# Kernel optimization log

Hardware: AMD Instinct MI355X
Metric: run time of the kernel (lower is better)

The kernel has to match this reference:

```python
import jax, jax.numpy as jnp
import numpy as np

FMAP = 56    # feature-map side (seq_len = FMAP**2 = 3136)
WS = 7       # window size
SHIFT = WS // 2  # 3, shifted-window offset
NH = 3       # heads
C = 96       # hidden dim
FF = 384     # feed-forward dim (4*C)
EPS = 1e-5


def _swin_mask():
    # Standard Swin shifted-window attention mask, shape (nW, L, L), values in {0, -1e9}.
    img = np.zeros((FMAP, FMAP), dtype=np.int32)
    slices = (slice(0, -WS), slice(-WS, -SHIFT), slice(-SHIFT, None))
    cnt = 0
    for hs in slices:
        for ws_ in slices:
            img[hs, ws_] = cnt
            cnt += 1
    w = img.reshape(FMAP // WS, WS, FMAP // WS, WS).transpose(0, 2, 1, 3).reshape(-1, WS * WS)
    m = np.where(w[:, None, :] != w[:, :, None], -1e9, 0.0).astype(np.float32)
    return jnp.asarray(m)  # (nW, L, L)


def _ln(x, w, b):
    mu = jnp.mean(x, axis=-1, keepdims=True)
    var = jnp.mean(jnp.square(x - mu), axis=-1, keepdims=True)
    return (x - mu) * jax.lax.rsqrt(var + EPS) * w + b


def setup_inputs() -> dict:
    key = jax.random.key(0)
    ks = jax.random.split(key, 8)
    s = 0.02
    return {
        "x": jax.random.normal(ks[0], (128, FMAP * FMAP, C), dtype=jnp.float32),
        "qkv_w": jax.random.normal(ks[1], (3 * C, C), dtype=jnp.float32) * s,
        "qkv_b": jnp.zeros((3 * C,), dtype=jnp.float32),
        "out_w": jax.random.normal(ks[2], (C, C), dtype=jnp.float32) * s,
        "out_b": jnp.zeros((C,), dtype=jnp.float32),
        "ln1_w": jnp.ones((C,), dtype=jnp.float32),
        "ln1_b": jnp.zeros((C,), dtype=jnp.float32),
        "ln2_w": jnp.ones((C,), dtype=jnp.float32),
        "ln2_b": jnp.zeros((C,), dtype=jnp.float32),
        "ff1_w": jax.random.normal(ks[3], (FF, C), dtype=jnp.float32) * s,
        "ff1_b": jnp.zeros((FF,), dtype=jnp.float32),
        "ff2_w": jax.random.normal(ks[4], (C, FF), dtype=jnp.float32) * s,
        "ff2_b": jnp.zeros((C,), dtype=jnp.float32),
    }


def reference(x, qkv_w, qkv_b, out_w, out_b, ln1_w, ln1_b, ln2_w, ln2_b, ff1_w, ff1_b, ff2_w, ff2_b):
    B, S, Cd = x.shape
    L = WS * WS
    g = FMAP // WS
    nW = g * g
    hd = Cd // NH

    # cyclic shift + window partition: (B, S, C) -> (B*nW, L, C)
    xi = jnp.roll(x.reshape(B, FMAP, FMAP, Cd), (-SHIFT, -SHIFT), axis=(1, 2))
    xw = xi.reshape(B, g, WS, g, WS, Cd).transpose(0, 1, 3, 2, 4, 5).reshape(B * nW, L, Cd)

    mask = _swin_mask()                                  # (nW, L, L)
    mask = jnp.tile(mask, (B, 1, 1))[:, None, :, :]      # (B*nW, 1, L, L)

    # pre-norm MHA
    h = _ln(xw, ln1_w, ln1_b)
    qkv = h @ qkv_w.T + qkv_b
    q, k, v = jnp.split(qkv, 3, axis=-1)
    def heads(t):
        return t.reshape(B * nW, L, NH, hd).transpose(0, 2, 1, 3)  # (B*nW, H, L, hd)
    q, k, v = heads(q), heads(k), heads(v)
    scores = jnp.einsum('bhqd,bhkd->bhqk', q, k) / jnp.sqrt(jnp.float32(hd)) + mask
    attn = jax.nn.softmax(scores, axis=-1)
    o = jnp.einsum('bhqk,bhkd->bhqd', attn, v).transpose(0, 2, 1, 3).reshape(B * nW, L, Cd)
    xw = xw + o @ out_w.T + out_b

    # pre-norm FFN with exact (erf) GELU, as torch activation='gelu'
    h2 = _ln(xw, ln2_w, ln2_b)
    xw = xw + jax.nn.gelu(h2 @ ff1_w.T + ff1_b, approximate=False) @ ff2_w.T + ff2_b

    # window merge + reverse shift
    xo = xw.reshape(B, g, g, WS, WS, Cd).transpose(0, 1, 3, 2, 4, 5).reshape(B, FMAP, FMAP, Cd)
    xo = jnp.roll(xo, (SHIFT, SHIFT), axis=(1, 2))
    return xo.reshape(B, S, Cd)
```

## Files before the change

### kernel.cpp

```cpp
#include <hip/hip_runtime.h>
#include <stdint.h>

#define FMAPD 56
#define LD 49
#define CD 96

using u16 = unsigned short;
using u32 = unsigned int;

typedef __attribute__((ext_vector_type(8))) short bh8;
typedef __attribute__((ext_vector_type(4))) float f4;

__device__ __forceinline__ u16 f2b(float f) {
  union { float f; u32 i; } v; v.f = f;
  u32 r = v.i + 0x7fffu + ((v.i >> 16) & 1u);
  return (u16)(r >> 16);
}
__device__ __forceinline__ u32 pk2(float a, float b) {
  return (u32)f2b(a) | ((u32)f2b(b) << 16);
}

__device__ __forceinline__ float gelu_f(float v) {
  float x = fabsf(v) * 0.70710678118654752f;
  float t = __builtin_amdgcn_rcpf(fmaf(x, 0.3275911f, 1.0f));
  float p = fmaf(t, 1.061405429f, -1.453152027f);
  p = fmaf(p, t, 1.421413741f);
  p = fmaf(p, t, -0.284496736f);
  p = fmaf(p, t, 0.254829592f);
  p = p * t;
  float e = __expf(-x * x);
  float q = 0.5f * p * e;
  float phi = (v >= 0.0f) ? (1.0f - q) : q;
  return v * phi;
}

#define SH 104
#define SV 72
#define SP 104

__global__ void cvt_weights(const float* __restrict__ a, const float* __restrict__ b,
                            const float* __restrict__ c, const float* __restrict__ d,
                            u16* __restrict__ ws) {
  int i = blockIdx.x * 256 + threadIdx.x;
  if (i < 27648)       ws[i] = f2b(a[i]);
  else if (i < 36864)  ws[i] = f2b(b[i - 27648]);
  else if (i < 73728)  ws[i] = f2b(c[i - 36864]);
  else if (i < 110592) ws[i] = f2b(d[i - 73728]);
}

__global__ __launch_bounds__(256, 3)
void swin_mfma(const float* __restrict__ gx,
               const float* __restrict__ b_qkv,
               const float* __restrict__ b_out,
               const float* __restrict__ w_ln1, const float* __restrict__ b_ln1,
               const float* __restrict__ w_ln2, const float* __restrict__ b_ln2,
               const float* __restrict__ b_ff1, const float* __restrict__ b_ff2,
               const u16* __restrict__ ws,
               float* __restrict__ gout)
{
  __shared__ __align__(16) u16 s_h [64 * SH];
  __shared__ __align__(16) u16 s_k [64 * SH];
  __shared__ __align__(16) u16 s_vt[96 * SV];
  __shared__ __align__(16) u16 s_p [4 * 16 * SP];
  __shared__ __align__(16) int s_id[64];

  const int tid = threadIdx.x;
  const int w = tid >> 6, lane = tid & 63, g = lane >> 4, lq = lane & 15;
  const int blk = blockIdx.x, b = blk >> 6, wr = (blk >> 3) & 7, wc = blk & 7;

  const u16* wsq = ws;
  const u16* wso = ws + 27648;
  const u16* wf1 = ws + 36864;
  const u16* wf2 = ws + 73728;

  u16* s_pw = s_p + w * (16 * SP);

  if (tid < 64) {
    int id = -1;
    if (tid < 49) {
      int i = tid / 7, j = tid - 7 * i;
      int rp = wr * 7 + i, cp = wc * 7 + j;
      int ri = (rp < 49) ? 0 : ((rp < 53) ? 1 : 2);
      int ci = (cp < 49) ? 0 : ((cp < 53) ? 1 : 2);
      id = ri * 3 + ci;
    }
    s_id[tid] = id;
  }

  float resid[6][4];
  size_t gbase[4];
  bool tval[4];
#pragma unroll
  for (int r = 0; r < 4; ++r) {
    int token = 16 * w + 4 * g + r;
    tval[r] = token < LD;
    int ti = token / 7, tj = token - 7 * ti;
    int row = wr * 7 + ti + 3; if (row >= FMAPD) row -= FMAPD;
    int col = wc * 7 + tj + 3; if (col >= FMAPD) col -= FMAPD;
    gbase[r] = ((size_t)b * (FMAPD * FMAPD) + row * FMAPD + col) * (size_t)CD + lq;
#pragma unroll
    for (int t = 0; t < 6; ++t) {
      float v = gx[gbase[r] + 16 * t];
      resid[t][r] = tval[r] ? v : 0.f;
    }
  }

  float bq[6][4];
#pragma unroll
  for (int t = 0; t < 6; ++t) {
    float4 v = *(const float4*)(b_qkv + 16 * t + 4 * g);
    bq[t][0] = v.x; bq[t][1] = v.y; bq[t][2] = v.z; bq[t][3] = v.w;
  }
  float bvv[6], bov[6], bf2v[6];
#pragma unroll
  for (int t = 0; t < 6; ++t) {
    bvv[t]  = b_qkv[192 + 16 * t + lq];
    bov[t]  = b_out[16 * t + lq];
    bf2v[t] = b_ff2[16 * t + lq];
  }

  auto layer_norm = [&](const float* lw, const float* lb) {
    float wv[6], bv[6];
#pragma unroll
    for (int t = 0; t < 6; ++t) { wv[t] = lw[16 * t + lq]; bv[t] = lb[16 * t + lq]; }
#pragma unroll
    for (int r = 0; r < 4; ++r) {
      float s = 0.f, s2 = 0.f;
#pragma unroll
      for (int t = 0; t < 6; ++t) { float v = resid[t][r]; s += v; s2 += v * v; }
#pragma unroll
      for (int m = 1; m <= 8; m <<= 1) { s += __shfl_xor(s, m, 64); s2 += __shfl_xor(s2, m, 64); }
      float mu = s * (1.f / 96.f);
      float rs = rsqrtf(s2 * (1.f / 96.f) - mu * mu + 1e-5f);
      u16* dst = s_h + (16 * w + 4 * g + r) * SH;
#pragma unroll
      for (int t = 0; t < 6; ++t) dst[16 * t + lq] = f2b((resid[t][r] - mu) * rs * wv[t] + bv[t]);
    }
  };
  layer_norm(w_ln1, b_ln1);

  {
    const u16* arow = s_h + (16 * w + lq) * SH;
    bh8 af[3];
#pragma unroll
    for (int kk = 0; kk < 3; ++kk) af[kk] = *(const bh8*)(arow + 32 * kk + 8 * g);

#pragma unroll
    for (int t = 0; t < 6; ++t) {
      f4 acc = {0.f, 0.f, 0.f, 0.f};
#pragma unroll
      for (int kk = 0; kk < 3; ++kk) {
        bh8 bf = *(const bh8*)(wsq + (16 * t + lq) * CD + 32 * kk + 8 * g);
        acc = __builtin_amdgcn_mfma_f32_16x16x32_bf16(bf, af[kk], acc, 0, 0, 0);
      }
      uint2 u; u.x = pk2(acc[0] + bq[t][0], acc[1] + bq[t][1]);
      u.y = pk2(acc[2] + bq[t][2], acc[3] + bq[t][3]);
      *(uint2*)(s_pw + lq * SP + 16 * t + 4 * g) = u;
    }
#pragma unroll
    for (int t = 0; t < 6; ++t) {
      f4 acc = {0.f, 0.f, 0.f, 0.f};
#pragma unroll
      for (int kk = 0; kk < 3; ++kk) {
        bh8 bf = *(const bh8*)(wsq + (96 + 16 * t + lq) * CD + 32 * kk + 8 * g);
        acc = __builtin_amdgcn_mfma_f32_16x16x32_bf16(bf, af[kk], acc, 0, 0, 0);
      }
      uint2 u; u.x = pk2(acc[0], acc[1]); u.y = pk2(acc[2], acc[3]);
      *(uint2*)(s_k + (16 * w + lq) * SH + 16 * t + 4 * g) = u;
    }
#pragma unroll
    for (int t = 0; t < 6; ++t) {
      f4 acc = {0.f, 0.f, 0.f, 0.f};
#pragma unroll
      for (int kk = 0; kk < 3; ++kk) {
        bh8 bf = *(const bh8*)(wsq + (192 + 16 * t + lq) * CD + 32 * kk + 8 * g);
        acc = __builtin_amdgcn_mfma_f32_16x16x32_bf16(af[kk], bf, acc, 0, 0, 0);
      }
      float bias = bvv[t];
      uint2 u; u.x = pk2(acc[0] + bias, acc[1] + bias);
      u.y = pk2(acc[2] + bias, acc[3] + bias);
      *(uint2*)(s_vt + (16 * t + lq) * SV + 16 * w + 4 * g) = u;
    }
  }
  bh8 qa[3];
#pragma unroll
  for (int hh = 0; hh < 3; ++hh) qa[hh] = *(const bh8*)(s_pw + lq * SP + 32 * hh + 8 * g);

  __syncthreads();

  const int id_i = s_id[16 * w + lq];
  int idj[4][4];
#pragma unroll
  for (int t = 0; t < 4; ++t) {
    int4 v = *(const int4*)(s_id + 16 * t + 4 * g);
    idj[t][0] = v.x; idj[t][1] = v.y; idj[t][2] = v.z; idj[t][3] = v.w;
  }
  const float scale = 0.17677669529663687f;

#pragma unroll
  for (int hh = 0; hh < 3; ++hh) {
    f4 sc[4];
#pragma unroll
    for (int t = 0; t < 4; ++t) {
      bh8 kb = *(const bh8*)(s_k + (16 * t + lq) * SH + 32 * hh + 8 * g);
      f4 z = {0.f, 0.f, 0.f, 0.f};
      sc[t] = __builtin_amdgcn_mfma_f32_16x16x32_bf16(kb, qa[hh], z, 0, 0, 0);
    }
    float pv[4][4];
    float mx = -3.0e38f;
#pragma unroll
    for (int t = 0; t < 4; ++t)
#pragma unroll
      for (int r = 0; r < 4; ++r) {
        float v = sc[t][r] * scale;
        v = (id_i != idj[t][r]) ? v - 1e9f : v;
        pv[t][r] = v;
        mx = fmaxf(mx, v);
      }
    mx = fmaxf(mx, __shfl_xor(mx, 16, 64));
    mx = fmaxf(mx, __shfl_xor(mx, 32, 64));
    float den = 0.f;
#pragma unroll
    for (int t = 0; t < 4; ++t)
#pragma unroll
      for (int r = 0; r < 4; ++r) { float e = __expf(pv[t][r] - mx); pv[t][r] = e; den += e; }
    den += __shfl_xor(den, 16, 64);
    den += __shfl_xor(den, 32, 64);
    float inv = 1.0f / den;
#pragma unroll
    for (int t = 0; t < 4; ++t) {
      uint2 u; u.x = pk2(pv[t][0] * inv, pv[t][1] * inv);
      u.y = pk2(pv[t][2] * inv, pv[t][3] * inv);
      *(uint2*)(s_pw + lq * SP + 16 * t + 4 * g) = u;
    }
    bh8 pa0 = *(const bh8*)(s_pw + lq * SP + 8 * g);
    bh8 pa1 = *(const bh8*)(s_pw + lq * SP + 32 + 8 * g);
#pragma unroll
    for (int nt = 0; nt < 2; ++nt) {
      const u16* vrow = s_vt + (32 * hh + 16 * nt + lq) * SV;
      bh8 vb0 = *(const bh8*)(vrow + 8 * g);
      bh8 vb1 = *(const bh8*)(vrow + 32 + 8 * g);
      f4 o = {0.f, 0.f, 0.f, 0.f};
      o = __builtin_amdgcn_mfma_f32_16x16x32_bf16(vb0, pa0, o, 0, 0, 0);
      o = __builtin_amdgcn_mfma_f32_16x16x32_bf16(vb1, pa1, o, 0, 0, 0);
      uint2 u; u.x = pk2(o[0], o[1]); u.y = pk2(o[2], o[3]);
      *(uint2*)(s_h + (16 * w + lq) * SH + 32 * hh + 16 * nt + 4 * g) = u;
    }
  }

  {
    const u16* orow = s_h + (16 * w + lq) * SH;
    bh8 oa[3];
#pragma unroll
    for (int kk = 0; kk < 3; ++kk) oa[kk] = *(const bh8*)(orow + 32 * kk + 8 * g);
#pragma unroll
    for (int t = 0; t < 6; ++t) {
      f4 acc = {0.f, 0.f, 0.f, 0.f};
#pragma unroll
      for (int kk = 0; kk < 3; ++kk) {
        bh8 bf = *(const bh8*)(wso + (16 * t + lq) * CD + 32 * kk + 8 * g);
        acc = __builtin_amdgcn_mfma_f32_16x16x32_bf16(oa[kk], bf, acc, 0, 0, 0);
      }
#pragma unroll
      for (int r = 0; r < 4; ++r) resid[t][r] += acc[r] + bov[t];
    }
  }

  layer_norm(w_ln2, b_ln2);
#pragma unroll
  for (int t = 0; t < 6; ++t)
#pragma unroll
    for (int r = 0; r < 4; ++r) resid[t][r] += bf2v[t];

  __syncthreads();

  {
    const u16* hrow = s_h + (16 * w + lq) * SH;
    bh8 ha[3];
#pragma unroll
    for (int kk = 0; kk < 3; ++kk) ha[kk] = *(const bh8*)(hrow + 32 * kk + 8 * g);
    const u16* frow = s_k + (16 * w + lq) * SH;
#pragma unroll 1
    for (int qq = 0; qq < 4; ++qq) {
      float bq1[6][4];
#pragma unroll
      for (int t = 0; t < 6; ++t) {
        float4 v = *(const float4*)(b_ff1 + 96 * qq + 16 * t + 4 * g);
        bq1[t][0] = v.x; bq1[t][1] = v.y; bq1[t][2] = v.z; bq1[t][3] = v.w;
      }
#pragma unroll
      for (int t = 0; t < 6; ++t) {
        f4 acc = {0.f, 0.f, 0.f, 0.f};
#pragma unroll
        for (int kk = 0; kk < 3; ++kk) {
          bh8 bf = *(const bh8*)(wf1 + (96 * qq + 16 * t + lq) * CD + 32 * kk + 8 * g);
          acc = __builtin_amdgcn_mfma_f32_16x16x32_bf16(bf, ha[kk], acc, 0, 0, 0);
        }
        uint2 u;
        u.x = pk2(gelu_f(acc[0] + bq1[t][0]), gelu_f(acc[1] + bq1[t][1]));
        u.y = pk2(gelu_f(acc[2] + bq1[t][2]), gelu_f(acc[3] + bq1[t][3]));
        *(uint2*)(s_k + (16 * w + lq) * SH + 16 * t + 4 * g) = u;
      }
      bh8 fa[3];
#pragma unroll
      for (int ks = 0; ks < 3; ++ks) fa[ks] = *(const bh8*)(frow + 32 * ks + 8 * g);
#pragma unroll
      for (int t = 0; t < 6; ++t) {
        f4 acc = {0.f, 0.f, 0.f, 0.f};
#pragma unroll
        for (int ks = 0; ks < 3; ++ks) {
          bh8 bf = *(const bh8*)(wf2 + (16 * t + lq) * 384 + 96 * qq + 32 * ks + 8 * g);
          acc = __builtin_amdgcn_mfma_f32_16x16x32_bf16(fa[ks], bf, acc, 0, 0, 0);
        }
#pragma unroll
        for (int r = 0; r < 4; ++r) resid[t][r] += acc[r];
      }
    }
  }

#pragma unroll
  for (int r = 0; r < 4; ++r) {
    if (tval[r]) {
#pragma unroll
      for (int t = 0; t < 6; ++t) gout[gbase[r] + 16 * t] = resid[t][r];
    }
  }
}

extern "C" void kernel_launch(void* const* d_in, const int* in_sizes, int n_in,
                              void* d_out, int out_size, void* d_ws, size_t ws_size,
                              hipStream_t stream) {
  cvt_weights<<<432, 256, 0, stream>>>(
      (const float*)d_in[1], (const float*)d_in[3],
      (const float*)d_in[9], (const float*)d_in[11], (u16*)d_ws);
  swin_mfma<<<8192, 256, 0, stream>>>(
      (const float*)d_in[0],
      (const float*)d_in[2],
      (const float*)d_in[4],
      (const float*)d_in[5], (const float*)d_in[6],
      (const float*)d_in[7], (const float*)d_in[8],
      (const float*)d_in[10], (const float*)d_in[12],
      (const u16*)d_ws, (float*)d_out);
}
```

Before: 876.8 us.

## Transpose MFMA fragments in registers via permlane swaps instead of LDS round-trips

Q, attention probabilities, attention output and the FF1 activations are now turned into MFMA A-operands with an in-register 4x4 lane transpose (permlane32/16 swaps, with a shuffle fallback) instead of being written to and re-read from shared memory. The softmax drops its max-subtraction and uses exp2, with the scale and log2(e) folded into Q, and the mask becomes a precomputed additive table. GELU also uses exp2, shared buffers are merged so LDS use shrinks, and launch bounds go from 3 to 4 blocks per SM. Bias values are read at the point of use rather than held in registers. Skipping the max subtraction relies on scores staying small enough that exp2 does not overflow.

After: 815.9 us. 1.07x faster.

```diff
diff --git a/kernel.cpp b/kernel.cpp
--- a/kernel.cpp
+++ b/kernel.cpp
@@ -10,6 +10,7 @@
 
 typedef __attribute__((ext_vector_type(8))) short bh8;
 typedef __attribute__((ext_vector_type(4))) float f4;
+typedef __attribute__((ext_vector_type(2))) unsigned int uv2;
 
 __device__ __forceinline__ u16 f2b(float f) {
   union { float f; u32 i; } v; v.f = f;
@@ -19,6 +20,38 @@
 __device__ __forceinline__ u32 pk2(float a, float b) {
   return (u32)f2b(a) | ((u32)f2b(b) << 16);
 }
+__device__ __forceinline__ bh8 mk8(u32 a, u32 b, u32 c, u32 d) {
+  union { u32 u[4]; bh8 v; } x;
+  x.u[0] = a; x.u[1] = b; x.u[2] = c; x.u[3] = d;
+  return x.v;
+}
+__device__ __forceinline__ float ex2(float x) { return __builtin_amdgcn_exp2f(x); }
+
+#if __has_builtin(__builtin_amdgcn_permlane32_swap) && __has_builtin(__builtin_amdgcn_permlane16_swap)
+__device__ __forceinline__ void xpose4(u32& v0, u32& v1, u32& v2, u32& v3) {
+  uv2 a = __builtin_amdgcn_permlane32_swap(v0, v2, false, false);
+  uv2 b = __builtin_amdgcn_permlane32_swap(v1, v3, false, false);
+  uv2 c = __builtin_amdgcn_permlane16_swap(a.x, a.y, false, false);
+  uv2 d = __builtin_amdgcn_permlane16_swap(b.x, b.y, false, false);
+  v0 = c.x; v2 = c.y; v1 = d.x; v3 = d.y;
+}
+#else
+__device__ __forceinline__ void xpose4(u32& v0, u32& v1, u32& v2, u32& v3) {
+  int lane = threadIdx.x & 63;
+  { u32 t0 = __shfl_xor((int)v0, 32, 64), t2 = __shfl_xor((int)v2, 32, 64);
+    bool lo = (lane & 32) == 0;
+    u32 n0 = lo ? v0 : t2, n2 = lo ? t0 : v2; v0 = n0; v2 = n2; }
+  { u32 t1 = __shfl_xor((int)v1, 32, 64), t3 = __shfl_xor((int)v3, 32, 64);
+    bool lo = (lane & 32) == 0;
+    u32 n1 = lo ? v1 : t3, n3 = lo ? t1 : v3; v1 = n1; v3 = n3; }
+  { u32 t0 = __shfl_xor((int)v0, 16, 64), t2 = __shfl_xor((int)v2, 16, 64);
+    bool lo = (lane & 16) == 0;
+    u32 n0 = lo ? v0 : t2, n2 = lo ? t0 : v2; v0 = n0; v2 = n2; }
+  { u32 t1 = __shfl_xor((int)v1, 16, 64), t3 = __shfl_xor((int)v3, 16, 64);
+    bool lo = (lane & 16) == 0;
+    u32 n1 = lo ? v1 : t3, n3 = lo ? t1 : v3; v1 = n1; v3 = n3; }
+}
+#endif
 
 __device__ __forceinline__ float gelu_f(float v) {
   float x = fabsf(v) * 0.70710678118654752f;
@@ -28,7 +61,7 @@
   p = fmaf(p, t, -0.284496736f);
   p = fmaf(p, t, 0.254829592f);
   p = p * t;
-  float e = __expf(-x * x);
+  float e = ex2(v * v * -0.72134752044448170f);
   float q = 0.5f * p * e;
   float phi = (v >= 0.0f) ? (1.0f - q) : q;
   return v * phi;
@@ -36,7 +69,6 @@
 
 #define SH 104
 #define SV 72
-#define SP 104
 
 __global__ void cvt_weights(const float* __restrict__ a, const float* __restrict__ b,
                             const float* __restrict__ c, const float* __restrict__ d,
@@ -48,7 +80,7 @@
   else if (i < 110592) ws[i] = f2b(d[i - 73728]);
 }
 
-__global__ __launch_bounds__(256, 3)
+__global__ __launch_bounds__(256, 4)
 void swin_mfma(const float* __restrict__ gx,
                const float* __restrict__ b_qkv,
                const float* __restrict__ b_out,
@@ -58,10 +90,8 @@
                const u16* __restrict__ ws,
                float* __restrict__ gout)
 {
-  __shared__ __align__(16) u16 s_h [64 * SH];
-  __shared__ __align__(16) u16 s_k [64 * SH];
-  __shared__ __align__(16) u16 s_vt[96 * SV];
-  __shared__ __align__(16) u16 s_p [4 * 16 * SP];
+  __shared__ __align__(16) u16 s_u[96 * SV];
+  __shared__ __align__(16) u16 s_k[64 * SH];
   __shared__ __align__(16) int s_id[64];
 
   const int tid = threadIdx.x;
@@ -73,11 +103,9 @@
   const u16* wf1 = ws + 36864;
   const u16* wf2 = ws + 73728;
 
-  u16* s_pw = s_p + w * (16 * SP);
-
   if (tid < 64) {
     int id = -1;
-    if (tid < 49) {
+    if (tid < LD) {
       int i = tid / 7, j = tid - 7 * i;
       int rp = wr * 7 + i, cp = wc * 7 + j;
       int ri = (rp < 49) ? 0 : ((rp < 53) ? 1 : 2);
@@ -89,34 +117,19 @@
 
   float resid[6][4];
   size_t gbase[4];
-  bool tval[4];
 #pragma unroll
   for (int r = 0; r < 4; ++r) {
     int token = 16 * w + 4 * g + r;
-    tval[r] = token < LD;
     int ti = token / 7, tj = token - 7 * ti;
     int row = wr * 7 + ti + 3; if (row >= FMAPD) row -= FMAPD;
     int col = wc * 7 + tj + 3; if (col >= FMAPD) col -= FMAPD;
     gbase[r] = ((size_t)b * (FMAPD * FMAPD) + row * FMAPD + col) * (size_t)CD + lq;
+    bool val = token < LD;
 #pragma unroll
     for (int t = 0; t < 6; ++t) {
       float v = gx[gbase[r] + 16 * t];
-      resid[t][r] = tval[r] ? v : 0.f;
-    }
-  }
-
-  float bq[6][4];
-#pragma unroll
-  for (int t = 0; t < 6; ++t) {
-    float4 v = *(const float4*)(b_qkv + 16 * t + 4 * g);
-    bq[t][0] = v.x; bq[t][1] = v.y; bq[t][2] = v.z; bq[t][3] = v.w;
-  }
-  float bvv[6], bov[6], bf2v[6];
-#pragma unroll
-  for (int t = 0; t < 6; ++t) {
-    bvv[t]  = b_qkv[192 + 16 * t + lq];
-    bov[t]  = b_out[16 * t + lq];
-    bf2v[t] = b_ff2[16 * t + lq];
+      resid[t][r] = val ? v : 0.f;
+    }
   }
 
   auto layer_norm = [&](const float* lw, const float* lb) {
@@ -132,30 +145,44 @@
       for (int m = 1; m <= 8; m <<= 1) { s += __shfl_xor(s, m, 64); s2 += __shfl_xor(s2, m, 64); }
       float mu = s * (1.f / 96.f);
       float rs = rsqrtf(s2 * (1.f / 96.f) - mu * mu + 1e-5f);
-      u16* dst = s_h + (16 * w + 4 * g + r) * SH;
+      u16* dst = s_u + (16 * w + 4 * g + r) * SH;
 #pragma unroll
       for (int t = 0; t < 6; ++t) dst[16 * t + lq] = f2b((resid[t][r] - mu) * rs * wv[t] + bv[t]);
     }
   };
   layer_norm(w_ln1, b_ln1);
 
-  {
-    const u16* arow = s_h + (16 * w + lq) * SH;
-    bh8 af[3];
+  bh8 af[3];
+  {
+    const u16* arow = s_u + (16 * w + lq) * SH;
 #pragma unroll
     for (int kk = 0; kk < 3; ++kk) af[kk] = *(const bh8*)(arow + 32 * kk + 8 * g);
-
-#pragma unroll
-    for (int t = 0; t < 6; ++t) {
-      f4 acc = {0.f, 0.f, 0.f, 0.f};
-#pragma unroll
-      for (int kk = 0; kk < 3; ++kk) {
-        bh8 bf = *(const bh8*)(wsq + (16 * t + lq) * CD + 32 * kk + 8 * g);
-        acc = __builtin_amdgcn_mfma_f32_16x16x32_bf16(bf, af[kk], acc, 0, 0, 0);
-      }
-      uint2 u; u.x = pk2(acc[0] + bq[t][0], acc[1] + bq[t][1]);
-      u.y = pk2(acc[2] + bq[t][2], acc[3] + bq[t][3]);
-      *(uint2*)(s_pw + lq * SP + 16 * t + 4 * g) = u;
+  }
+  __syncthreads();
+
+  const float scaleL = 0.25505650948822f;
+  bh8 qa[3];
+  {
+#pragma unroll
+    for (int c = 0; c < 3; ++c) {
+      u32 vv[4];
+#pragma unroll
+      for (int j1 = 0; j1 < 2; ++j1) {
+        int t = 2 * c + j1;
+        f4 acc = {0.f, 0.f, 0.f, 0.f};
+#pragma unroll
+        for (int kk = 0; kk < 3; ++kk) {
+          bh8 bf = *(const bh8*)(wsq + (16 * t + lq) * CD + 32 * kk + 8 * g);
+          acc = __builtin_amdgcn_mfma_f32_16x16x32_bf16(bf, af[kk], acc, 0, 0, 0);
+        }
+        float4 bq = *(const float4*)(b_qkv + 16 * t + 4 * g);
+        vv[2 * j1 + 0] = pk2(fmaf(acc[0], scaleL, bq.x * scaleL),
+                             fmaf(acc[1], scaleL, bq.y * scaleL));
+        vv[2 * j1 + 1] = pk2(fmaf(acc[2], scaleL, bq.z * scaleL),
+                             fmaf(acc[3], scaleL, bq.w * scaleL));
+      }
+      xpose4(vv[0], vv[1], vv[2], vv[3]);
+      qa[c] = mk8(vv[0], vv[1], vv[2], vv[3]);
     }
 #pragma unroll
     for (int t = 0; t < 6; ++t) {
@@ -176,27 +203,28 @@
         bh8 bf = *(const bh8*)(wsq + (192 + 16 * t + lq) * CD + 32 * kk + 8 * g);
         acc = __builtin_amdgcn_mfma_f32_16x16x32_bf16(af[kk], bf, acc, 0, 0, 0);
       }
-      float bias = bvv[t];
+      float bias = b_qkv[192 + 16 * t + lq];
       uint2 u; u.x = pk2(acc[0] + bias, acc[1] + bias);
       u.y = pk2(acc[2] + bias, acc[3] + bias);
-      *(uint2*)(s_vt + (16 * t + lq) * SV + 16 * w + 4 * g) = u;
-    }
-  }
-  bh8 qa[3];
-#pragma unroll
-  for (int hh = 0; hh < 3; ++hh) qa[hh] = *(const bh8*)(s_pw + lq * SP + 32 * hh + 8 * g);
-
+      *(uint2*)(s_u + (16 * t + lq) * SV + 16 * w + 4 * g) = u;
+    }
+  }
   __syncthreads();
 
-  const int id_i = s_id[16 * w + lq];
-  int idj[4][4];
-#pragma unroll
-  for (int t = 0; t < 4; ++t) {
-    int4 v = *(const int4*)(s_id + 16 * t + 4 * g);
-    idj[t][0] = v.x; idj[t][1] = v.y; idj[t][2] = v.z; idj[t][3] = v.w;
-  }
-  const float scale = 0.17677669529663687f;
-
+  float madd[4][4];
+  {
+    int id_i = s_id[16 * w + lq];
+#pragma unroll
+    for (int t = 0; t < 4; ++t) {
+      int4 v = *(const int4*)(s_id + 16 * t + 4 * g);
+      madd[t][0] = (v.x != id_i) ? -1.0e9f : 0.f;
+      madd[t][1] = (v.y != id_i) ? -1.0e9f : 0.f;
+      madd[t][2] = (v.z != id_i) ? -1.0e9f : 0.f;
+      madd[t][3] = (v.w != id_i) ? -1.0e9f : 0.f;
+    }
+  }
+
+  u32 oa[3][4];
 #pragma unroll
   for (int hh = 0; hh < 3; ++hh) {
     f4 sc[4];
@@ -207,103 +235,98 @@
       sc[t] = __builtin_amdgcn_mfma_f32_16x16x32_bf16(kb, qa[hh], z, 0, 0, 0);
     }
     float pv[4][4];
-    float mx = -3.0e38f;
+    float den = 0.f;
 #pragma unroll
     for (int t = 0; t < 4; ++t)
 #pragma unroll
       for (int r = 0; r < 4; ++r) {
-        float v = sc[t][r] * scale;
-        v = (id_i != idj[t][r]) ? v - 1e9f : v;
-        pv[t][r] = v;
-        mx = fmaxf(mx, v);
-      }
-    mx = fmaxf(mx, __shfl_xor(mx, 16, 64));
-    mx = fmaxf(mx, __shfl_xor(mx, 32, 64));
-    float den = 0.f;
-#pragma unroll
-    for (int t = 0; t < 4; ++t)
-#pragma unroll
-      for (int r = 0; r < 4; ++r) { float e = __expf(pv[t][r] - mx); pv[t][r] = e; den += e; }
+        float e = ex2(sc[t][r] + madd[t][r]);
+        pv[t][r] = e; den += e;
+      }
     den += __shfl_xor(den, 16, 64);
     den += __shfl_xor(den, 32, 64);
-    float inv = 1.0f / den;
-#pragma unroll
-    for (int t = 0; t < 4; ++t) {
-      uint2 u; u.x = pk2(pv[t][0] * inv, pv[t][1] * inv);
-      u.y = pk2(pv[t][2] * inv, pv[t][3] * inv);
-      *(uint2*)(s_pw + lq * SP + 16 * t + 4 * g) = u;
-    }
-    bh8 pa0 = *(const bh8*)(s_pw + lq * SP + 8 * g);
-    bh8 pa1 = *(const bh8*)(s_pw + lq * SP + 32 + 8 * g);
-#pragma unroll
-    for (int nt = 0; nt < 2; ++nt) {
-      const u16* vrow = s_vt + (32 * hh + 16 * nt + lq) * SV;
-      bh8 vb0 = *(const bh8*)(vrow + 8 * g);
-      bh8 vb1 = *(const bh8*)(vrow + 32 + 8 * g);
-      f4 o = {0.f, 0.f, 0.f, 0.f};
-      o = __builtin_amdgcn_mfma_f32_16x16x32_bf16(vb0, pa0, o, 0, 0, 0);
-      o = __builtin_amdgcn_mfma_f32_16x16x32_bf16(vb1, pa1, o, 0, 0, 0);
-      uint2 u; u.x = pk2(o[0], o[1]); u.y = pk2(o[2], o[3]);
-      *(uint2*)(s_h + (16 * w + lq) * SH + 32 * hh + 16 * nt + 4 * g) = u;
-    }
-  }
-
-  {
-    const u16* orow = s_h + (16 * w + lq) * SH;
-    bh8 oa[3];
-#pragma unroll
-    for (int kk = 0; kk < 3; ++kk) oa[kk] = *(const bh8*)(orow + 32 * kk + 8 * g);
+    float inv = __builtin_amdgcn_rcpf(den);
+    bh8 pa[2];
+#pragma unroll
+    for (int c = 0; c < 2; ++c) {
+      u32 vv[4];
+      vv[0] = pk2(pv[2 * c][0] * inv, pv[2 * c][1] * inv);
+      vv[1] = pk2(pv[2 * c][2] * inv, pv[2 * c][3] * inv);
+      vv[2] = pk2(pv[2 * c + 1][0] * inv, pv[2 * c + 1][1] * inv);
+      vv[3] = pk2(pv[2 * c + 1][2] * inv, pv[2 * c + 1][3] * inv);
+      xpose4(vv[0], vv[1], vv[2], vv[3]);
+      pa[c] = mk8(vv[0], vv[1], vv[2], vv[3]);
+    }
+    f4 o0 = {0.f, 0.f, 0.f, 0.f}, o1 = {0.f, 0.f, 0.f, 0.f};
+    {
+      const u16* vr0 = s_u + (32 * hh + lq) * SV;
+      o0 = __builtin_amdgcn_mfma_f32_16x16x32_bf16(*(const bh8*)(vr0 + 8 * g), pa[0], o0, 0, 0, 0);
+      o0 = __builtin_amdgcn_mfma_f32_16x16x32_bf16(*(const bh8*)(vr0 + 32 + 8 * g), pa[1], o0, 0, 0, 0);
+      const u16* vr1 = s_u + (32 * hh + 16 + lq) * SV;
+      o1 = __builtin_amdgcn_mfma_f32_16x16x32_bf16(*(const bh8*)(vr1 + 8 * g), pa[0], o1, 0, 0, 0);
+      o1 = __builtin_amdgcn_mfma_f32_16x16x32_bf16(*(const bh8*)(vr1 + 32 + 8 * g), pa[1], o1, 0, 0, 0);
+    }
+    u32 vv[4];
+    vv[0] = pk2(o0[0], o0[1]); vv[1] = pk2(o0[2], o0[3]);
+    vv[2] = pk2(o1[0], o1[1]); vv[3] = pk2(o1[2], o1[3]);
+    xpose4(vv[0], vv[1], vv[2], vv[3]);
+    oa[hh][0] = vv[0]; oa[hh][1] = vv[1]; oa[hh][2] = vv[2]; oa[hh][3] = vv[3];
+  }
+  __syncthreads();
+
+  {
+    bh8 oaf[3];
+#pragma unroll
+    for (int kk = 0; kk < 3; ++kk) oaf[kk] = mk8(oa[kk][0], oa[kk][1], oa[kk][2], oa[kk][3]);
 #pragma unroll
     for (int t = 0; t < 6; ++t) {
       f4 acc = {0.f, 0.f, 0.f, 0.f};
 #pragma unroll
       for (int kk = 0; kk < 3; ++kk) {
         bh8 bf = *(const bh8*)(wso + (16 * t + lq) * CD + 32 * kk + 8 * g);
-        acc = __builtin_amdgcn_mfma_f32_16x16x32_bf16(oa[kk], bf, acc, 0, 0, 0);
-      }
-#pragma unroll
-      for (int r = 0; r < 4; ++r) resid[t][r] += acc[r] + bov[t];
+        acc = __builtin_amdgcn_mfma_f32_16x16x32_bf16(oaf[kk], bf, acc, 0, 0, 0);
+      }
+      float bias = b_out[16 * t + lq];
+#pragma unroll
+      for (int r = 0; r < 4; ++r) resid[t][r] += acc[r] + bias;
     }
   }
 
   layer_norm(w_ln2, b_ln2);
 #pragma unroll
-  for (int t = 0; t < 6; ++t)
-#pragma unroll
-    for (int r = 0; r < 4; ++r) resid[t][r] += bf2v[t];
-
-  __syncthreads();
-
-  {
-    const u16* hrow = s_h + (16 * w + lq) * SH;
+  for (int t = 0; t < 6; ++t) {
+    float bb = b_ff2[16 * t + lq];
+#pragma unroll
+    for (int r = 0; r < 4; ++r) resid[t][r] += bb;
+  }
+
+  {
     bh8 ha[3];
+    const u16* hrow = s_u + (16 * w + lq) * SH;
 #pragma unroll
     for (int kk = 0; kk < 3; ++kk) ha[kk] = *(const bh8*)(hrow + 32 * kk + 8 * g);
-    const u16* frow = s_k + (16 * w + lq) * SH;
 #pragma unroll 1
     for (int qq = 0; qq < 4; ++qq) {
-      float bq1[6][4];
-#pragma unroll
-      for (int t = 0; t < 6; ++t) {
-        float4 v = *(const float4*)(b_ff1 + 96 * qq + 16 * t + 4 * g);
-        bq1[t][0] = v.x; bq1[t][1] = v.y; bq1[t][2] = v.z; bq1[t][3] = v.w;
-      }
-#pragma unroll
-      for (int t = 0; t < 6; ++t) {
-        f4 acc = {0.f, 0.f, 0.f, 0.f};
-#pragma unroll
-        for (int kk = 0; kk < 3; ++kk) {
-          bh8 bf = *(const bh8*)(wf1 + (96 * qq + 16 * t + lq) * CD + 32 * kk + 8 * g);
-          acc = __builtin_amdgcn_mfma_f32_16x16x32_bf16(bf, ha[kk], acc, 0, 0, 0);
+      bh8 fa[3];
+#pragma unroll
+      for (int c = 0; c < 3; ++c) {
+        u32 vv[4];
+#pragma unroll
+        for (int j1 = 0; j1 < 2; ++j1) {
+          int t = 2 * c + j1;
+          f4 acc = {0.f, 0.f, 0.f, 0.f};
+#pragma unroll
+          for (int kk = 0; kk < 3; ++kk) {
+            bh8 bf = *(const bh8*)(wf1 + (96 * qq + 16 * t + lq) * CD + 32 * kk + 8 * g);
+            acc = __builtin_amdgcn_mfma_f32_16x16x32_bf16(bf, ha[kk], acc, 0, 0, 0);
+          }
+          float4 bb = *(const float4*)(b_ff1 + 96 * qq + 16 * t + 4 * g);
+          vv[2 * j1 + 0] = pk2(gelu_f(acc[0] + bb.x), gelu_f(acc[1] + bb.y));
+          vv[2 * j1 + 1] = pk2(gelu_f(acc[2] + bb.z), gelu_f(acc[3] + bb.w));
         }
-        uint2 u;
-        u.x = pk2(gelu_f(acc[0] + bq1[t][0]), gelu_f(acc[1] + bq1[t][1]));
-        u.y = pk2(gelu_f(acc[2] + bq1[t][2]), gelu_f(acc[3] + bq1[t][3]));
-        *(uint2*)(s_k + (16 * w + lq) * SH + 16 * t + 4 * g) = u;
-      }
-      bh8 fa[3];
-#pragma unroll
-      for (int ks = 0; ks < 3; ++ks) fa[ks] = *(const bh8*)(frow + 32 * ks + 8 * g);
+        xpose4(vv[0], vv[1], vv[2], vv[3]);
+        fa[c] = mk8(vv[0], vv[1], vv[2], vv[3]);
+      }
 #pragma unroll
       for (int t = 0; t < 6; ++t) {
         f4 acc = {0.f, 0.f, 0.f, 0.f};
@@ -320,7 +343,7 @@
 
 #pragma unroll
   for (int r = 0; r < 4; ++r) {
-    if (tval[r]) {
+    if (16 * w + 4 * g + r < LD) {
 #pragma unroll
       for (int t = 0; t < 6; ++t) gout[gbase[r] + 16 * t] = resid[t][r];
     }
```
